# Kernel tuning notes

Hardware: AMD Instinct MI355X
Metric: run time of the kernel (lower is better)

Reference implementation:

```python
import jax, jax.numpy as jnp
import numpy as np

D_MODEL = 1024
NUM_HEADS = 16
HEAD_DIM = D_MODEL // NUM_HEADS


def setup_inputs() -> dict:
    key = jax.random.key(0)
    ks = jax.random.split(key, 12)
    B, S = 2, 2048
    scale = 1.0 / np.sqrt(D_MODEL)
    inp = {
        "x": jax.random.normal(ks[0], (B, S, D_MODEL), dtype=jnp.float32),
        "docking_scores": jax.random.uniform(ks[1], (B, S), dtype=jnp.float32),
        "q_w": jax.random.normal(ks[2], (D_MODEL, D_MODEL), dtype=jnp.float32) * scale,
        "q_b": jnp.zeros((D_MODEL,), dtype=jnp.float32),
        "k_w": jax.random.normal(ks[3], (D_MODEL, D_MODEL), dtype=jnp.float32) * scale,
        "k_b": jnp.zeros((D_MODEL,), dtype=jnp.float32),
        "v_w": jax.random.normal(ks[4], (D_MODEL, D_MODEL), dtype=jnp.float32) * scale,
        "v_b": jnp.zeros((D_MODEL,), dtype=jnp.float32),
        "o_w": jax.random.normal(ks[5], (D_MODEL, D_MODEL), dtype=jnp.float32) * scale,
        "o_b": jnp.zeros((D_MODEL,), dtype=jnp.float32),
        "alpha": jnp.float32(0.5),
    }
    return inp


def reference(x, docking_scores, q_w, q_b, k_w, k_b, v_w, v_b, o_w, o_b, alpha):
    B, S, _ = x.shape
    # Projections; weights stored as (in, out) so y = x @ W + b
    def proj(w, b):
        y = jnp.einsum('bsd,de->bse', x, w) + b
        return y.reshape(B, S, NUM_HEADS, HEAD_DIM).transpose(0, 2, 1, 3)  # (B,H,S,hd)
    Q = proj(q_w, q_b)
    K = proj(k_w, k_b)
    V = proj(v_w, v_b)
    scores = jnp.einsum('bhqd,bhkd->bhqk', Q, K) / np.sqrt(HEAD_DIM)
    attn = jax.nn.softmax(scores, axis=-1)  # (B,H,S,S)
    # post-softmax docking blend, broadcast over heads and query positions
    ds = docking_scores[:, None, None, :]  # (B,1,1,S)
    attn = (1.0 - alpha) * attn + alpha * ds
    ctx = jnp.einsum('bhqk,bhkd->bhqd', attn, V)
    ctx = ctx.transpose(0, 2, 1, 3).reshape(B, S, D_MODEL)
    return jnp.einsum('bsd,de->bse', ctx, o_w) + o_b
```

## Files before the change

kernel.cpp:

```cpp
#include <hip/hip_runtime.h>
#include <hip/hip_bf16.h>

typedef __attribute__((ext_vector_type(8)))  short bf16x8;
typedef __attribute__((ext_vector_type(4)))  float f32x4;
typedef __attribute__((ext_vector_type(16))) float f32x16;
typedef __attribute__((ext_vector_type(4)))  int   i32x4;
typedef __attribute__((ext_vector_type(4)))  unsigned short u16x4;
typedef __attribute__((ext_vector_type(8)))  unsigned short u16x8;

__device__ __forceinline__ unsigned short f2bf(float f) {
    unsigned int u = __builtin_bit_cast(unsigned int, f);
    u += 0x7FFFu + ((u >> 16) & 1u);
    return (unsigned short)(u >> 16);
}
__device__ __forceinline__ float bf2f(unsigned short h) {
    unsigned int u = ((unsigned int)h) << 16;
    return __builtin_bit_cast(float, u);
}
__device__ __forceinline__ bf16x8 ld16(const unsigned short* p) {
    return *reinterpret_cast<const bf16x8*>(p);
}
__device__ __forceinline__ float fexp2(float x) {
    float r; asm("v_exp_f32 %0, %1" : "=v"(r) : "v"(x)); return r;
}
__device__ __forceinline__ float frcp(float x) {
    float r; asm("v_rcp_f32 %0, %1" : "=v"(r) : "v"(x)); return r;
}
__device__ __forceinline__ void pswap(unsigned int& a, unsigned int& b) {
    asm("v_permlane32_swap_b32 %0, %1" : "+v"(a), "+v"(b));
}

__global__ void cvt_x_kernel(const float* __restrict__ in, unsigned short* __restrict__ out, int n8) {
    int idx = blockIdx.x * blockDim.x + threadIdx.x;
    int stride = gridDim.x * blockDim.x;
    for (int i = idx; i < n8; i += stride) {
        f32x4 a = reinterpret_cast<const f32x4*>(in)[i*2];
        f32x4 b = reinterpret_cast<const f32x4*>(in)[i*2+1];
        u16x8 o;
        o[0]=f2bf(a[0]); o[1]=f2bf(a[1]); o[2]=f2bf(a[2]); o[3]=f2bf(a[3]);
        o[4]=f2bf(b[0]); o[5]=f2bf(b[1]); o[6]=f2bf(b[2]); o[7]=f2bf(b[3]);
        reinterpret_cast<u16x8*>(out)[i] = o;
    }
}

__global__ void tr_w_kernel(const float* __restrict__ q_w, const float* __restrict__ k_w,
                            const float* __restrict__ v_w, const float* __restrict__ o_w,
                            unsigned short* __restrict__ WT) {
    __shared__ float tile[32][33];
    const float* W = (blockIdx.z == 0) ? q_w : (blockIdx.z == 1) ? k_w : (blockIdx.z == 2) ? v_w : o_w;
    unsigned short* dst = WT + (size_t)blockIdx.z * 1024 * 1024;
    int tx = threadIdx.x, ty = threadIdx.y;
    int n0 = blockIdx.x * 32, k0 = blockIdx.y * 32;
#pragma unroll
    for (int j = 0; j < 4; ++j)
        tile[ty + j*8][tx] = W[(size_t)(k0 + ty + j*8) * 1024 + n0 + tx];
    __syncthreads();
#pragma unroll
    for (int j = 0; j < 4; ++j)
        dst[(size_t)(n0 + ty + j*8) * 1024 + k0 + tx] = f2bf(tile[tx][ty + j*8]);
}

__global__ __launch_bounds__(256) void gemm_qkv(
    const unsigned short* __restrict__ A,
    const unsigned short* __restrict__ WT,
    const float* __restrict__ qb, const float* __restrict__ kbias, const float* __restrict__ vbias,
    unsigned short* __restrict__ Qo, unsigned short* __restrict__ Ko, unsigned short* __restrict__ Vto)
{
    __shared__ __align__(16) unsigned short As[2][128*64];
    __shared__ __align__(16) unsigned short Bs[2][128*64];
    const int tid = threadIdx.x, lane = tid & 63, w = tid >> 6;
    const int wm = w >> 1, wn = w & 1;
    const int m0 = blockIdx.y * 128, n0 = blockIdx.x * 128;
    const int K = 1024;
    const int sr = tid >> 3, ssl = tid & 7;
    const int ssw = (ssl ^ (sr & 7)) << 3;
    f32x4 acc[4][4] = {};

    auto stage = [&](int buf, int k0) {
#pragma unroll
        for (int j = 0; j < 4; ++j) {
            const int c = j*256 + tid, r = j*32 + sr;
            __builtin_amdgcn_global_load_lds(
                (const __attribute__((address_space(1))) void*)&A[(size_t)(m0+r)*K + k0 + ssw],
                (__attribute__((address_space(3))) void*)&As[buf][(size_t)c*8], 16, 0, 0);
            __builtin_amdgcn_global_load_lds(
                (const __attribute__((address_space(1))) void*)&WT[(size_t)(n0+r)*K + k0 + ssw],
                (__attribute__((address_space(3))) void*)&Bs[buf][(size_t)c*8], 16, 0, 0);
        }
    };

    stage(0, 0);
#pragma unroll 1
    for (int t = 0; t < 16; ++t) {
        __syncthreads();
        if (t < 15) stage((t + 1) & 1, (t + 1) * 64);
        const unsigned short* pa = &As[t & 1][0];
        const unsigned short* pb = &Bs[t & 1][0];
#pragma unroll
        for (int kc = 0; kc < 2; ++kc) {
            bf16x8 af[4], bfr[4];
            const int slog = kc*4 + (lane >> 4);
#pragma unroll
            for (int t2 = 0; t2 < 4; ++t2) {
                const int row = wm*64 + t2*16 + (lane & 15);
                af[t2]  = ld16(&pa[row*64 + ((slog ^ (row & 7)) << 3)]);
                const int col = wn*64 + t2*16 + (lane & 15);
                bfr[t2] = ld16(&pb[col*64 + ((slog ^ (col & 7)) << 3)]);
            }
#pragma unroll
            for (int mt = 0; mt < 4; ++mt)
#pragma unroll
                for (int nt = 0; nt < 4; ++nt)
                    acc[mt][nt] = __builtin_amdgcn_mfma_f32_16x16x32_bf16(af[mt], bfr[nt], acc[mt][nt], 0, 0, 0);
        }
    }
    const int mat = n0 >> 10;
    if (mat == 2) {
#pragma unroll
        for (int mt = 0; mt < 4; ++mt)
#pragma unroll
        for (int nt = 0; nt < 4; ++nt) {
            const int nl = (n0 & 1023) + wn*64 + nt*16 + (lane & 15);
            const int h = nl >> 6, hd = nl & 63;
            const int mbase = m0 + wm*64 + mt*16 + ((lane >> 4) << 2);
            const int b = mbase >> 11, s = mbase & 2047;
            const float bv = vbias[nl];
            u16x4 pk;
#pragma unroll
            for (int r = 0; r < 4; ++r) pk[r] = f2bf(acc[mt][nt][r] + bv);
            *reinterpret_cast<u16x4*>(&Vto[((size_t)((b << 4) | h) * 64 + hd) * 2048 + s]) = pk;
        }
    } else {
        unsigned short* outp = mat ? Ko : Qo;
        const float* bias = mat ? kbias : qb;
        const float scale = mat ? 1.0f : 0.180336881f;
#pragma unroll
        for (int mt = 0; mt < 4; ++mt)
#pragma unroll
        for (int nt = 0; nt < 4; ++nt) {
            const int nl = (n0 & 1023) + wn*64 + nt*16 + (lane & 15);
            const int h = nl >> 6, hd = nl & 63;
            const int mbase = m0 + wm*64 + mt*16 + ((lane >> 4) << 2);
            const float bv = bias[nl];
#pragma unroll
            for (int r = 0; r < 4; ++r) {
                const int mm2 = mbase + r, b = mm2 >> 11, s = mm2 & 2047;
                outp[((size_t)((b << 4) | h) * 2048 + s) * 64 + hd] = f2bf((acc[mt][nt][r] + bv) * scale);
            }
        }
    }
}

__global__ __launch_bounds__(256) void gemm_o(
    const unsigned short* __restrict__ A, const unsigned short* __restrict__ WT,
    const float* __restrict__ bias, float* __restrict__ Cout)
{
    __shared__ __align__(16) unsigned short As[2][128*64];
    __shared__ __align__(16) unsigned short Bs[2][128*64];
    const int tid = threadIdx.x, lane = tid & 63, w = tid >> 6;
    const int wm = w >> 1, wn = w & 1;
    const int m0 = blockIdx.y * 128, n0 = blockIdx.x * 128;
    const int K = 1024;
    const int sr = tid >> 3, ssl = tid & 7;
    const int ssw = (ssl ^ (sr & 7)) << 3;
    f32x4 acc[4][4] = {};

    auto stage = [&](int buf, int k0) {
#pragma unroll
        for (int j = 0; j < 4; ++j) {
            const int c = j*256 + tid, r = j*32 + sr;
            __builtin_amdgcn_global_load_lds(
                (const __attribute__((address_space(1))) void*)&A[(size_t)(m0+r)*K + k0 + ssw],
                (__attribute__((address_space(3))) void*)&As[buf][(size_t)c*8], 16, 0, 0);
            __builtin_amdgcn_global_load_lds(
                (const __attribute__((address_space(1))) void*)&WT[(size_t)(n0+r)*K + k0 + ssw],
                (__attribute__((address_space(3))) void*)&Bs[buf][(size_t)c*8], 16, 0, 0);
        }
    };

    stage(0, 0);
#pragma unroll 1
    for (int t = 0; t < 16; ++t) {
        __syncthreads();
        if (t < 15) stage((t + 1) & 1, (t + 1) * 64);
        const unsigned short* pa = &As[t & 1][0];
        const unsigned short* pb = &Bs[t & 1][0];
#pragma unroll
        for (int kc = 0; kc < 2; ++kc) {
            bf16x8 af[4], bfr[4];
            const int slog = kc*4 + (lane >> 4);
#pragma unroll
            for (int t2 = 0; t2 < 4; ++t2) {
                const int row = wm*64 + t2*16 + (lane & 15);
                af[t2]  = ld16(&pa[row*64 + ((slog ^ (row & 7)) << 3)]);
                const int col = wn*64 + t2*16 + (lane & 15);
                bfr[t2] = ld16(&pb[col*64 + ((slog ^ (col & 7)) << 3)]);
            }
#pragma unroll
            for (int mt = 0; mt < 4; ++mt)
#pragma unroll
                for (int nt = 0; nt < 4; ++nt)
                    acc[mt][nt] = __builtin_amdgcn_mfma_f32_16x16x32_bf16(af[mt], bfr[nt], acc[mt][nt], 0, 0, 0);
        }
    }
#pragma unroll
    for (int mt = 0; mt < 4; ++mt)
#pragma unroll
    for (int nt = 0; nt < 4; ++nt) {
        const int n = n0 + wn*64 + nt*16 + (lane & 15);
        const int mbase = m0 + wm*64 + mt*16 + ((lane >> 4) << 2);
        const float bv = bias[n];
#pragma unroll
        for (int r = 0; r < 4; ++r)
            Cout[(size_t)(mbase + r) * 1024 + n] = acc[mt][nt][r] + bv;
    }
}

__global__ void dock_c_kernel(const float* __restrict__ ds, const unsigned short* __restrict__ Vt,
                              float* __restrict__ cvec) {
    __shared__ float red[256];
    const int bh = blockIdx.x >> 3, sl = blockIdx.x & 7;
    const int b = bh >> 4;
    const int t = threadIdx.x, d = t & 63, q4 = t >> 6;
    const unsigned short* vrow = &Vt[(size_t)bh * 131072 + (size_t)d * 2048 + sl * 256 + q4 * 64];
    const float* dsr = &ds[b * 2048 + sl * 256 + q4 * 64];
    float sum = 0.f;
#pragma unroll
    for (int k = 0; k < 64; k += 8) {
        bf16x8 v = ld16(&vrow[k]);
#pragma unroll
        for (int i = 0; i < 8; ++i) sum += dsr[k + i] * bf2f((unsigned short)v[i]);
    }
    red[t] = sum;
    __syncthreads();
    if (t < 64) atomicAdd(&cvec[bh * 64 + t], red[t] + red[64 + t] + red[128 + t] + red[192 + t]);
}

__global__ __launch_bounds__(256, 2) void attn_kernel(
    const unsigned short* __restrict__ Qp,
    const unsigned short* __restrict__ Kp,
    const unsigned short* __restrict__ Vp,
    const float* __restrict__ cvec,
    const float* __restrict__ alpha_p,
    unsigned short* __restrict__ ctx)
{
    __shared__ __align__(16) unsigned short Ks[2][4096];
    __shared__ __align__(16) unsigned short Vs[2][4096];
    __shared__ float sml[4][32];
    const int tid = threadIdx.x, lane = tid & 63, w = tid >> 6;
    const int hi = lane >> 5, ln = lane & 31;
    const int wg = blockIdx.x;
    const int swz = (wg & 7) * 64 + (wg >> 3);
    const int bh = swz >> 4, qt = swz & 15;
    const int q0 = qt * 128 + w * 32;
    const size_t hb = (size_t)bh * (2048 * 64);
    const float alpha = *alpha_p;

    const int sr = tid >> 3, ss = tid & 7;
    const int ssw = (ss ^ (sr & 7)) << 3;
    const unsigned short* Kg = Kp + hb;
    const unsigned short* Vg = Vp + hb;

    bf16x8 qf[4];
    {
        const unsigned short* qr = &Qp[hb + (size_t)(q0 + ln) * 64 + hi * 8];
#pragma unroll
        for (int ks = 0; ks < 4; ++ks) qf[ks] = ld16(qr + ks * 16);
    }

    const short one_bf = (short)0x3F80;
    const bf16x8 onesf = {one_bf, one_bf, one_bf, one_bf, one_bf, one_bf, one_bf, one_bf};

    f32x16 oacc0 = {}, oacc1 = {}, lacc = {};
    float m = -1e30f;

    auto stage = [&](int buf, int it) {
#pragma unroll
        for (int p = 0; p < 2; ++p) {
            __builtin_amdgcn_global_load_lds(
                (const __attribute__((address_space(1))) void*)&Kg[(size_t)(it*64 + p*32 + sr) * 64 + ssw],
                (__attribute__((address_space(3))) void*)&Ks[buf][p*2048 + tid*8], 16, 0, 0);
            __builtin_amdgcn_global_load_lds(
                (const __attribute__((address_space(1))) void*)&Vg[(size_t)(p*32 + sr) * 2048 + it*64 + ssw],
                (__attribute__((address_space(3))) void*)&Vs[buf][p*2048 + tid*8], 16, 0, 0);
        }
    };

    bf16x8 kf[8];
    auto ldk = [&](const unsigned short* base) {
#pragma unroll
        for (int t2 = 0; t2 < 2; ++t2)
#pragma unroll
        for (int ks = 0; ks < 4; ++ks) {
            const int row = t2*32 + ln;
            const int sl  = ((ks*2 + hi) ^ (row & 7)) << 3;
            kf[t2*4+ks] = ld16(base + row*64 + sl);
        }
    };

    stage(0, 0);
    __syncthreads();
    stage(1, 1);
    ldk(&Ks[0][0]);
    f32x16 sA0 = {}, sA1 = {}, sB0 = {}, sB1 = {};
#pragma unroll
    for (int ks = 0; ks < 4; ++ks) {
        sA0 = __builtin_amdgcn_mfma_f32_32x32x16_bf16(kf[ks],   qf[ks], sA0, 0, 0, 0);
        sA1 = __builtin_amdgcn_mfma_f32_32x32x16_bf16(kf[4+ks], qf[ks], sA1, 0, 0, 0);
    }

    auto step = [&](f32x16& sc0, f32x16& sc1, f32x16& sn0, f32x16& sn1, int buf, int it) {
        bf16x8 vf[8];
#pragma unroll
        for (int t2 = 0; t2 < 2; ++t2)
#pragma unroll
        for (int ks = 0; ks < 4; ++ks) {
            const int row = t2*32 + ln;
            const int sl  = ((ks*2 + hi) ^ (row & 7)) << 3;
            vf[t2*4+ks] = ld16(&Vs[buf][row*64 + sl]);
        }
        __syncthreads();
        if (it + 2 < 32) stage(buf, it + 2);
        const bool more = (it + 1 < 32);
        if (more) ldk(&Ks[buf ^ 1][0]);
        __builtin_amdgcn_s_setprio(1);
        if (more) {
            sn0 = {}; sn1 = {};
#pragma unroll
            for (int ks = 0; ks < 4; ++ks) {
                sn0 = __builtin_amdgcn_mfma_f32_32x32x16_bf16(kf[ks],   qf[ks], sn0, 0, 0, 0);
                sn1 = __builtin_amdgcn_mfma_f32_32x32x16_bf16(kf[4+ks], qf[ks], sn1, 0, 0, 0);
            }
        }
        float mx[8];
#pragma unroll
        for (int r = 0; r < 8; ++r)
            mx[r] = fmaxf(fmaxf(sc0[r], sc0[r+8]), fmaxf(sc1[r], sc1[r+8]));
        float tm = fmaxf(fmaxf(fmaxf(mx[0],mx[1]), fmaxf(mx[2],mx[3])),
                         fmaxf(fmaxf(mx[4],mx[5]), fmaxf(mx[6],mx[7])));
        {
            unsigned int ua = __builtin_bit_cast(unsigned int, tm), ub = ua;
            pswap(ua, ub);
            tm = fmaxf(__builtin_bit_cast(float, ua), __builtin_bit_cast(float, ub));
        }
        if (__any(tm > m + 8.f)) {
            float mn = fmaxf(m, tm);
            float sc = fexp2(m - mn);
            m = mn;
            if (hi == 0) sml[w][ln] = sc;
#pragma unroll
            for (int m4 = 0; m4 < 4; ++m4) {
                f32x4 sv = *reinterpret_cast<const f32x4*>(&sml[w][m4*8 + hi*4]);
#pragma unroll
                for (int r3 = 0; r3 < 4; ++r3) {
                    oacc0[m4*4+r3] *= sv[r3];
                    oacc1[m4*4+r3] *= sv[r3];
                    lacc [m4*4+r3] *= sv[r3];
                }
            }
        }
        float p0a[16], p1a[16];
#pragma unroll
        for (int r = 0; r < 16; ++r) {
            p0a[r] = fexp2(sc0[r] - m);
            p1a[r] = fexp2(sc1[r] - m);
        }

        unsigned int Wp0[4][2], Wp1[4][2];
#pragma unroll
        for (int m4 = 0; m4 < 4; ++m4)
#pragma unroll
        for (int jj = 0; jj < 2; ++jj) {
            asm("v_cvt_pk_bf16_f32 %0, %1, %2" : "=v"(Wp0[m4][jj]) : "v"(p0a[m4*4+jj*2]), "v"(p0a[m4*4+jj*2+1]));
            asm("v_cvt_pk_bf16_f32 %0, %1, %2" : "=v"(Wp1[m4][jj]) : "v"(p1a[m4*4+jj*2]), "v"(p1a[m4*4+jj*2+1]));
        }
#pragma unroll
        for (int ks = 0; ks < 4; ++ks) {
            const int tp = ks & 1;
            unsigned int a0, a1, b0, b1;
            if (ks < 2) { a0 = Wp0[2*tp][0]; a1 = Wp0[2*tp][1]; b0 = Wp0[2*tp+1][0]; b1 = Wp0[2*tp+1][1]; }
            else        { a0 = Wp1[2*tp][0]; a1 = Wp1[2*tp][1]; b0 = Wp1[2*tp+1][0]; b1 = Wp1[2*tp+1][1]; }
            pswap(a0, b0);
            pswap(a1, b1);
            i32x4 pw;
            pw[0] = (int)a0; pw[1] = (int)a1; pw[2] = (int)b0; pw[3] = (int)b1;
            bf16x8 pf = __builtin_bit_cast(bf16x8, pw);
            oacc0 = __builtin_amdgcn_mfma_f32_32x32x16_bf16(pf, vf[ks],   oacc0, 0, 0, 0);
            oacc1 = __builtin_amdgcn_mfma_f32_32x32x16_bf16(pf, vf[4+ks], oacc1, 0, 0, 0);
            lacc  = __builtin_amdgcn_mfma_f32_32x32x16_bf16(pf, onesf,    lacc,  0, 0, 0);
        }
        __builtin_amdgcn_s_setprio(0);
    };

#pragma unroll 1
    for (int ii = 0; ii < 16; ++ii) {
        step(sA0, sA1, sB0, sB1, 0, ii*2);
        step(sB0, sB1, sA0, sA1, 1, ii*2 + 1);
    }

    const int b = bh >> 4, h = bh & 15;
    const float a1f = 1.f - alpha;
    const float cv0 = alpha * cvec[bh*64 + ln];
    const float cv1 = alpha * cvec[bh*64 + 32 + ln];
#pragma unroll
    for (int m4 = 0; m4 < 4; ++m4) {
#pragma unroll
        for (int r3 = 0; r3 < 4; ++r3) {
            const int row = m4*8 + hi*4 + r3;
            const int s = q0 + row;
            const float iv = frcp(lacc[m4*4 + r3]);
            unsigned short* orow = &ctx[((size_t)(b*2048 + s))*1024 + h*64 + ln];
            orow[0]  = f2bf(a1f * oacc0[m4*4+r3] * iv + cv0);
            orow[32] = f2bf(a1f * oacc1[m4*4+r3] * iv + cv1);
        }
    }
}

extern "C" void kernel_launch(void* const* d_in, const int* in_sizes, int n_in,
                              void* d_out, int out_size, void* d_ws, size_t ws_size,
                              hipStream_t stream) {
    const float* x     = (const float*)d_in[0];
    const float* ds    = (const float*)d_in[1];
    const float* q_w   = (const float*)d_in[2];
    const float* q_b   = (const float*)d_in[3];
    const float* k_w   = (const float*)d_in[4];
    const float* k_b   = (const float*)d_in[5];
    const float* v_w   = (const float*)d_in[6];
    const float* v_b   = (const float*)d_in[7];
    const float* o_w   = (const float*)d_in[8];
    const float* o_b   = (const float*)d_in[9];
    const float* alpha = (const float*)d_in[10];

    char* ws = (char*)d_ws;
    const size_t MB = 1024 * 1024;
    unsigned short* xb   = (unsigned short*)(ws);
    unsigned short* wT   = (unsigned short*)(ws + 8  * MB);
    unsigned short* Qb   = (unsigned short*)(ws + 16 * MB);
    unsigned short* Kb   = (unsigned short*)(ws + 24 * MB);
    unsigned short* Vt   = (unsigned short*)(ws + 32 * MB);
    float*          cvec = (float*)         (ws + 40 * MB);
    unsigned short* ctxb = xb;

    const int M = 4096, K = 1024;

    cvt_x_kernel<<<2048, 256, 0, stream>>>(x, xb, M * K / 8);

    dim3 tb(32, 8);
    dim3 tg(32, 32, 4);
    tr_w_kernel<<<tg, tb, 0, stream>>>(q_w, k_w, v_w, o_w, wT);

    dim3 gqkv(24, 32);
    gemm_qkv<<<gqkv, 256, 0, stream>>>(xb, wT, q_b, k_b, v_b, Qb, Kb, Vt);

    hipMemsetAsync(cvec, 0, 32 * 64 * sizeof(float), stream);
    dock_c_kernel<<<256, 256, 0, stream>>>(ds, Vt, cvec);

    attn_kernel<<<512, 256, 0, stream>>>(Qb, Kb, Vt, cvec, alpha, ctxb);

    dim3 go(8, 32);
    gemm_o<<<go, 256, 0, stream>>>(ctxb, wT + (size_t)3 * MB, o_b, (float*)d_out);
}
```

Baseline: 127.7 us.

## Store K and V in MFMA fragment order and load them directly from global

The QKV GEMM epilogue now writes K and V in a pre-swizzled layout that matches the MFMA operand fragments. The attention kernel then reads K/V fragments straight from global memory into registers, dropping the LDS staging, the barriers and the double buffering. The next K fragment is register-prefetched while softmax runs. The docking-vector kernel is rewritten for the new V layout with one block per head, which removes the memset and the atomics. The trade-off is that every wave loads K/V from global/L2 on its own with no LDS sharing, which raises global traffic and exposes load latency. The scattered K writes in the GEMM epilogue are also less coalesced.

```diff
diff --git a/kernel.cpp b/kernel.cpp
--- a/kernel.cpp
+++ b/kernel.cpp
@@ -60,11 +60,12 @@
         dst[(size_t)(n0 + ty + j*8) * 1024 + k0 + tx] = f2bf(tile[tx][ty + j*8]);
 }
 
+
 __global__ __launch_bounds__(256) void gemm_qkv(
     const unsigned short* __restrict__ A,
     const unsigned short* __restrict__ WT,
     const float* __restrict__ qb, const float* __restrict__ kbias, const float* __restrict__ vbias,
-    unsigned short* __restrict__ Qo, unsigned short* __restrict__ Ko, unsigned short* __restrict__ Vto)
+    unsigned short* __restrict__ Qo, unsigned short* __restrict__ KFo, unsigned short* __restrict__ VFo)
 {
     __shared__ __align__(16) unsigned short As[2][128*64];
     __shared__ __align__(16) unsigned short Bs[2][128*64];
@@ -128,12 +129,11 @@
             u16x4 pk;
 #pragma unroll
             for (int r = 0; r < 4; ++r) pk[r] = f2bf(acc[mt][nt][r] + bv);
-            *reinterpret_cast<u16x4*>(&Vto[((size_t)((b << 4) | h) * 64 + hd) * 2048 + s]) = pk;
-        }
-    } else {
-        unsigned short* outp = mat ? Ko : Qo;
-        const float* bias = mat ? kbias : qb;
-        const float scale = mat ? 1.0f : 0.180336881f;
+            const size_t off = (size_t)((b << 4) | h) * 131072 + (s >> 6) * 4096 + (hd >> 5) * 2048
+                             + ((s >> 4) & 3) * 512 + ((s >> 3) & 1) * 256 + (hd & 31) * 8 + (s & 7);
+            *reinterpret_cast<u16x4*>(&VFo[off]) = pk;
+        }
+    } else if (mat == 1) {
 #pragma unroll
         for (int mt = 0; mt < 4; ++mt)
 #pragma unroll
@@ -141,11 +141,29 @@
             const int nl = (n0 & 1023) + wn*64 + nt*16 + (lane & 15);
             const int h = nl >> 6, hd = nl & 63;
             const int mbase = m0 + wm*64 + mt*16 + ((lane >> 4) << 2);
-            const float bv = bias[nl];
+            const float bv = kbias[nl];
 #pragma unroll
             for (int r = 0; r < 4; ++r) {
                 const int mm2 = mbase + r, b = mm2 >> 11, s = mm2 & 2047;
-                outp[((size_t)((b << 4) | h) * 2048 + s) * 64 + hd] = f2bf((acc[mt][nt][r] + bv) * scale);
+                const size_t off = (size_t)((b << 4) | h) * 131072 + (s >> 5) * 2048 + (hd >> 4) * 512
+                                 + ((hd >> 3) & 1) * 256 + (s & 31) * 8 + (hd & 7);
+                KFo[off] = f2bf(acc[mt][nt][r] + bv);
+            }
+        }
+    } else {
+        const float scale = 0.180336881f;
+#pragma unroll
+        for (int mt = 0; mt < 4; ++mt)
+#pragma unroll
+        for (int nt = 0; nt < 4; ++nt) {
+            const int nl = (n0 & 1023) + wn*64 + nt*16 + (lane & 15);
+            const int h = nl >> 6, hd = nl & 63;
+            const int mbase = m0 + wm*64 + mt*16 + ((lane >> 4) << 2);
+            const float bv = qb[nl];
+#pragma unroll
+            for (int r = 0; r < 4; ++r) {
+                const int mm2 = mbase + r, b = mm2 >> 11, s = mm2 & 2047;
+                Qo[((size_t)((b << 4) | h) * 2048 + s) * 64 + hd] = f2bf((acc[mt][nt][r] + bv) * scale);
             }
         }
     }
@@ -216,36 +234,47 @@
     }
 }
 
-__global__ void dock_c_kernel(const float* __restrict__ ds, const unsigned short* __restrict__ Vt,
+__global__ void dock_c_kernel(const float* __restrict__ ds, const unsigned short* __restrict__ VF,
                               float* __restrict__ cvec) {
     __shared__ float red[256];
-    const int bh = blockIdx.x >> 3, sl = blockIdx.x & 7;
+    const int bh = blockIdx.x;
     const int b = bh >> 4;
-    const int t = threadIdx.x, d = t & 63, q4 = t >> 6;
-    const unsigned short* vrow = &Vt[(size_t)bh * 131072 + (size_t)d * 2048 + sl * 256 + q4 * 64];
-    const float* dsr = &ds[b * 2048 + sl * 256 + q4 * 64];
+    const int t = threadIdx.x;
+    const int lane = t & 63, t2 = (t >> 6) & 1, k4 = t >> 7;
+    const int hi = lane >> 5;
+    const unsigned short* VFb = VF + (size_t)bh * 131072;
+    const float* dsb = ds + b * 2048;
     float sum = 0.f;
-#pragma unroll
-    for (int k = 0; k < 64; k += 8) {
-        bf16x8 v = ld16(&vrow[k]);
-#pragma unroll
-        for (int i = 0; i < 8; ++i) sum += dsr[k + i] * bf2f((unsigned short)v[i]);
+    for (int kvt = k4; kvt < 32; kvt += 2) {
+#pragma unroll
+        for (int ks = 0; ks < 4; ++ks) {
+            bf16x8 v = ld16(VFb + kvt*4096 + t2*2048 + ks*512 + lane*8);
+            const int kv0 = kvt*64 + ks*16 + hi*8;
+            f32x4 d0 = *reinterpret_cast<const f32x4*>(&dsb[kv0]);
+            f32x4 d1 = *reinterpret_cast<const f32x4*>(&dsb[kv0 + 4]);
+            sum += d0[0]*bf2f((unsigned short)v[0]) + d0[1]*bf2f((unsigned short)v[1])
+                 + d0[2]*bf2f((unsigned short)v[2]) + d0[3]*bf2f((unsigned short)v[3])
+                 + d1[0]*bf2f((unsigned short)v[4]) + d1[1]*bf2f((unsigned short)v[5])
+                 + d1[2]*bf2f((unsigned short)v[6]) + d1[3]*bf2f((unsigned short)v[7]);
+        }
     }
     red[t] = sum;
     __syncthreads();
-    if (t < 64) atomicAdd(&cvec[bh * 64 + t], red[t] + red[64 + t] + red[128 + t] + red[192 + t]);
+    if (t < 64) {
+        const int ln = t & 31, tt2 = t >> 5;
+        const int base = tt2 * 64 + ln;
+        cvec[bh * 64 + tt2 * 32 + ln] = red[base] + red[base + 32] + red[base + 128] + red[base + 160];
+    }
 }
 
 __global__ __launch_bounds__(256, 2) void attn_kernel(
     const unsigned short* __restrict__ Qp,
-    const unsigned short* __restrict__ Kp,
-    const unsigned short* __restrict__ Vp,
+    const unsigned short* __restrict__ KF,
+    const unsigned short* __restrict__ VF,
     const float* __restrict__ cvec,
     const float* __restrict__ alpha_p,
     unsigned short* __restrict__ ctx)
 {
-    __shared__ __align__(16) unsigned short Ks[2][4096];
-    __shared__ __align__(16) unsigned short Vs[2][4096];
     __shared__ float sml[4][32];
     const int tid = threadIdx.x, lane = tid & 63, w = tid >> 6;
     const int hi = lane >> 5, ln = lane & 31;
@@ -256,10 +285,8 @@
     const size_t hb = (size_t)bh * (2048 * 64);
     const float alpha = *alpha_p;
 
-    const int sr = tid >> 3, ss = tid & 7;
-    const int ssw = (ss ^ (sr & 7)) << 3;
-    const unsigned short* Kg = Kp + hb;
-    const unsigned short* Vg = Vp + hb;
+    const unsigned short* KFb = KF + (size_t)bh * 131072;
+    const unsigned short* VFb = VF + (size_t)bh * 131072;
 
     bf16x8 qf[4];
     {
@@ -274,64 +301,32 @@
     f32x16 oacc0 = {}, oacc1 = {}, lacc = {};
     float m = -1e30f;
 
-    auto stage = [&](int buf, int it) {
-#pragma unroll
-        for (int p = 0; p < 2; ++p) {
-            __builtin_amdgcn_global_load_lds(
-                (const __attribute__((address_space(1))) void*)&Kg[(size_t)(it*64 + p*32 + sr) * 64 + ssw],
-                (__attribute__((address_space(3))) void*)&Ks[buf][p*2048 + tid*8], 16, 0, 0);
-            __builtin_amdgcn_global_load_lds(
-                (const __attribute__((address_space(1))) void*)&Vg[(size_t)(p*32 + sr) * 2048 + it*64 + ssw],
-                (__attribute__((address_space(3))) void*)&Vs[buf][p*2048 + tid*8], 16, 0, 0);
-        }
+    auto ldk = [&](bf16x8 (&kf)[8], int it) {
+#pragma unroll
+        for (int t2 = 0; t2 < 2; ++t2)
+#pragma unroll
+        for (int ks = 0; ks < 4; ++ks)
+            kf[t2*4+ks] = ld16(KFb + (it*2 + t2)*2048 + ks*512 + lane*8);
     };
 
-    bf16x8 kf[8];
-    auto ldk = [&](const unsigned short* base) {
+    bf16x8 kfA[8], kfB[8];
+    ldk(kfA, 0);
+    f32x16 sA0 = {}, sA1 = {}, sB0 = {}, sB1 = {};
+#pragma unroll
+    for (int ks = 0; ks < 4; ++ks) {
+        sA0 = __builtin_amdgcn_mfma_f32_32x32x16_bf16(kfA[ks],   qf[ks], sA0, 0, 0, 0);
+        sA1 = __builtin_amdgcn_mfma_f32_32x32x16_bf16(kfA[4+ks], qf[ks], sA1, 0, 0, 0);
+    }
+
+    auto step = [&](f32x16& sc0, f32x16& sc1, f32x16& sn0, f32x16& sn1, bf16x8 (&kn)[8], int it) {
+        bf16x8 vf[8];
 #pragma unroll
         for (int t2 = 0; t2 < 2; ++t2)
 #pragma unroll
-        for (int ks = 0; ks < 4; ++ks) {
-            const int row = t2*32 + ln;
-            const int sl  = ((ks*2 + hi) ^ (row & 7)) << 3;
-            kf[t2*4+ks] = ld16(base + row*64 + sl);
-        }
-    };
-
-    stage(0, 0);
-    __syncthreads();
-    stage(1, 1);
-    ldk(&Ks[0][0]);
-    f32x16 sA0 = {}, sA1 = {}, sB0 = {}, sB1 = {};
-#pragma unroll
-    for (int ks = 0; ks < 4; ++ks) {
-        sA0 = __builtin_amdgcn_mfma_f32_32x32x16_bf16(kf[ks],   qf[ks], sA0, 0, 0, 0);
-        sA1 = __builtin_amdgcn_mfma_f32_32x32x16_bf16(kf[4+ks], qf[ks], sA1, 0, 0, 0);
-    }
-
-    auto step = [&](f32x16& sc0, f32x16& sc1, f32x16& sn0, f32x16& sn1, int buf, int it) {
-        bf16x8 vf[8];
-#pragma unroll
-        for (int t2 = 0; t2 < 2; ++t2)
-#pragma unroll
-        for (int ks = 0; ks < 4; ++ks) {
-            const int row = t2*32 + ln;
-            const int sl  = ((ks*2 + hi) ^ (row & 7)) << 3;
-            vf[t2*4+ks] = ld16(&Vs[buf][row*64 + sl]);
-        }
-        __syncthreads();
-        if (it + 2 < 32) stage(buf, it + 2);
+        for (int ks = 0; ks < 4; ++ks)
+            vf[t2*4+ks] = ld16(VFb + it*4096 + t2*2048 + ks*512 + lane*8);
         const bool more = (it + 1 < 32);
-        if (more) ldk(&Ks[buf ^ 1][0]);
-        __builtin_amdgcn_s_setprio(1);
-        if (more) {
-            sn0 = {}; sn1 = {};
-#pragma unroll
-            for (int ks = 0; ks < 4; ++ks) {
-                sn0 = __builtin_amdgcn_mfma_f32_32x32x16_bf16(kf[ks],   qf[ks], sn0, 0, 0, 0);
-                sn1 = __builtin_amdgcn_mfma_f32_32x32x16_bf16(kf[4+ks], qf[ks], sn1, 0, 0, 0);
-            }
-        }
+        if (more) ldk(kn, it + 1);
         float mx[8];
 #pragma unroll
         for (int r = 0; r < 8; ++r)
@@ -365,7 +360,6 @@
             p0a[r] = fexp2(sc0[r] - m);
             p1a[r] = fexp2(sc1[r] - m);
         }
-
         unsigned int Wp0[4][2], Wp1[4][2];
 #pragma unroll
         for (int m4 = 0; m4 < 4; ++m4)
@@ -373,6 +367,15 @@
         for (int jj = 0; jj < 2; ++jj) {
             asm("v_cvt_pk_bf16_f32 %0, %1, %2" : "=v"(Wp0[m4][jj]) : "v"(p0a[m4*4+jj*2]), "v"(p0a[m4*4+jj*2+1]));
             asm("v_cvt_pk_bf16_f32 %0, %1, %2" : "=v"(Wp1[m4][jj]) : "v"(p1a[m4*4+jj*2]), "v"(p1a[m4*4+jj*2+1]));
+        }
+        __builtin_amdgcn_s_setprio(1);
+        if (more) {
+            sn0 = {}; sn1 = {};
+#pragma unroll
+            for (int ks = 0; ks < 4; ++ks) {
+                sn0 = __builtin_amdgcn_mfma_f32_32x32x16_bf16(kn[ks],   qf[ks], sn0, 0, 0, 0);
+                sn1 = __builtin_amdgcn_mfma_f32_32x32x16_bf16(kn[4+ks], qf[ks], sn1, 0, 0, 0);
+            }
         }
 #pragma unroll
         for (int ks = 0; ks < 4; ++ks) {
@@ -394,8 +397,8 @@
 
 #pragma unroll 1
     for (int ii = 0; ii < 16; ++ii) {
-        step(sA0, sA1, sB0, sB1, 0, ii*2);
-        step(sB0, sB1, sA0, sA1, 1, ii*2 + 1);
+        step(sA0, sA1, sB0, sB1, kfB, ii*2);
+        step(sB0, sB1, sA0, sA1, kfA, ii*2 + 1);
     }
 
     const int b = bh >> 4, h = bh & 15;
@@ -436,8 +439,8 @@
     unsigned short* xb   = (unsigned short*)(ws);
     unsigned short* wT   = (unsigned short*)(ws + 8  * MB);
     unsigned short* Qb   = (unsigned short*)(ws + 16 * MB);
-    unsigned short* Kb   = (unsigned short*)(ws + 24 * MB);
-    unsigned short* Vt   = (unsigned short*)(ws + 32 * MB);
+    unsigned short* KFb  = (unsigned short*)(ws + 24 * MB);
+    unsigned short* VFb  = (unsigned short*)(ws + 32 * MB);
     float*          cvec = (float*)         (ws + 40 * MB);
     unsigned short* ctxb = xb;
 
@@ -450,12 +453,11 @@
     tr_w_kernel<<<tg, tb, 0, stream>>>(q_w, k_w, v_w, o_w, wT);
 
     dim3 gqkv(24, 32);
-    gemm_qkv<<<gqkv, 256, 0, stream>>>(xb, wT, q_b, k_b, v_b, Qb, Kb, Vt);
-
-    hipMemsetAsync(cvec, 0, 32 * 64 * sizeof(float), stream);
-    dock_c_kernel<<<256, 256, 0, stream>>>(ds, Vt, cvec);
-
-    attn_kernel<<<512, 256, 0, stream>>>(Qb, Kb, Vt, cvec, alpha, ctxb);
+    gemm_qkv<<<gqkv, 256, 0, stream>>>(xb, wT, q_b, k_b, v_b, Qb, KFb, VFb);
+
+    dock_c_kernel<<<32, 256, 0, stream>>>(ds, VFb, cvec);
+
+    attn_kernel<<<512, 256, 0, stream>>>(Qb, KFb, VFb, cvec, alpha, ctxb);
 
     dim3 go(8, 32);
     gemm_o<<<go, 256, 0, stream>>>(ctxb, wT + (size_t)3 * MB, o_b, (float*)d_out);
```

Result: slower. 141.7 us (+10.9%).
